# Kernel optimization log

Measured on AMD Instinct MI355X. Metric: run time of the kernel, lower is better.

Reference implementation:

```python
import jax, jax.numpy as jnp
import numpy as np
from jax import lax

N, C, K, M = 131072, 128, 27, 65536
EPS = 1e-5


def setup_inputs() -> dict:
    key = jax.random.key(0)
    ks = jax.random.split(key, 8)
    w_scale = 1.0 / np.sqrt(K * C)  # sane fan-in init for stacked kernel weights
    return {
        "x": jax.random.normal(ks[0], (N, C), jnp.float32),
        "W1": jax.random.normal(ks[1], (K, C, C), jnp.float32) * w_scale,
        "gamma1": jnp.ones((C,), jnp.float32),
        "beta1": jnp.zeros((C,), jnp.float32),
        "W2": jax.random.normal(ks[2], (K, C, C), jnp.float32) * w_scale,
        "gamma2": jnp.ones((C,), jnp.float32),
        "beta2": jnp.zeros((C,), jnp.float32),
        "map1_in": jax.random.randint(ks[3], (K, M), 0, N, jnp.int32),
        "map1_out": jax.random.randint(ks[4], (K, M), 0, N, jnp.int32),
        "map2_in": jax.random.randint(ks[5], (K, M), 0, N, jnp.int32),
        "map2_out": jax.random.randint(ks[6], (K, M), 0, N, jnp.int32),
    }


def sparse_conv(x, W, idx_in, idx_out):
    # gather-GEMM-scatter over K kernel offsets (Minkowski kernel map)
    def body(acc, kmap):
        w, ii, io = kmap                      # [C,C], [M], [M]
        contrib = x[ii] @ w                   # gather [M,C] then GEMM
        return acc.at[io].add(contrib), None  # scatter-add
    out, _ = lax.scan(body, jnp.zeros((x.shape[0], W.shape[-1]), x.dtype),
                      (W, idx_in, idx_out))
    return out


def batch_norm(x, gamma, beta):
    m = jnp.mean(x, axis=0)
    v = jnp.var(x, axis=0)
    return (x - m) * lax.rsqrt(v + EPS) * gamma + beta


def reference(x, W1, gamma1, beta1, W2, gamma2, beta2,
              map1_in, map1_out, map2_in, map2_out):
    residual = x
    out = sparse_conv(x, W1, map1_in, map1_out)
    out = jax.nn.elu(batch_norm(out, gamma1, beta1))
    out = sparse_conv(out, W2, map2_in, map2_out)
    out = batch_norm(out, gamma2, beta2) + residual
    return jax.nn.elu(out)
```

## Files before the change

kernel.cpp:

```cpp
#include <hip/hip_runtime.h>

typedef unsigned short u16;
typedef unsigned int u32;

#define NPTS 131072
#define CD 128
#define KOFF 27
#define MMAP 65536
#define LDAB 136
#define LDC 132

__device__ __forceinline__ u16 f2bf(float f) {
  u32 u = __float_as_uint(f);
  u32 r = (u + 0x7fffu + ((u >> 16) & 1u)) >> 16;
  return (u16)r;
}

typedef __attribute__((ext_vector_type(8))) short bf16x8;
typedef __attribute__((ext_vector_type(4))) float f32x4;

__global__ __launch_bounds__(256) void k_convert_x(const float* __restrict__ x,
                                                   u16* __restrict__ xb) {
  long i = ((long)blockIdx.x * 256 + threadIdx.x) * 8;
  float4 a = *(const float4*)(x + i);
  float4 b = *(const float4*)(x + i + 4);
  uint4 v;
  v.x = f2bf(a.x) | ((u32)f2bf(a.y) << 16);
  v.y = f2bf(a.z) | ((u32)f2bf(a.w) << 16);
  v.z = f2bf(b.x) | ((u32)f2bf(b.y) << 16);
  v.w = f2bf(b.z) | ((u32)f2bf(b.w) << 16);
  *(uint4*)(xb + i) = v;
}

__global__ __launch_bounds__(256) void k_convert_w(const float* __restrict__ W,
                                                   u16* __restrict__ Wb) {
  int idx = blockIdx.x * 256 + threadIdx.x;
  if (idx >= KOFF * 2048) return;
  int k = idx >> 11;
  int rem = idx & 2047;
  int co = rem >> 4;
  int cc = rem & 15;
  const float* ws = W + (long)k * (CD * CD) + (long)(cc * 8) * CD + co;
  u16 t[8];
#pragma unroll
  for (int j = 0; j < 8; ++j) t[j] = f2bf(ws[j * CD]);
  uint4 v;
  v.x = t[0] | ((u32)t[1] << 16);
  v.y = t[2] | ((u32)t[3] << 16);
  v.z = t[4] | ((u32)t[5] << 16);
  v.w = t[6] | ((u32)t[7] << 16);
  ((uint4*)Wb)[idx] = v;
}

__global__ __launch_bounds__(256) void k_hist(const int* __restrict__ mo,
                                              u32* __restrict__ hist) {
  int i = blockIdx.x * 256 + threadIdx.x;
  atomicAdd(&hist[mo[i]], 1u);
}

__global__ __launch_bounds__(256) void k_scanA(const u32* __restrict__ hist,
                                               u32* __restrict__ offs,
                                               u32* __restrict__ bsum) {
  __shared__ u32 sh[256];
  int t = threadIdx.x, b = blockIdx.x, i = b * 256 + t;
  u32 v = hist[i];
  u32 run = v;
  sh[t] = run;
  __syncthreads();
  for (int d = 1; d < 256; d <<= 1) {
    u32 y = (t >= d) ? sh[t - d] : 0u;
    __syncthreads();
    run += y;
    sh[t] = run;
    __syncthreads();
  }
  offs[i] = run - v;
  if (t == 255) bsum[b] = run;
}

__global__ __launch_bounds__(512) void k_scanB(u32* __restrict__ bsum) {
  __shared__ u32 sh[512];
  int t = threadIdx.x;
  u32 v = bsum[t];
  u32 run = v;
  sh[t] = run;
  __syncthreads();
  for (int d = 1; d < 512; d <<= 1) {
    u32 y = (t >= d) ? sh[t - d] : 0u;
    __syncthreads();
    run += y;
    sh[t] = run;
    __syncthreads();
  }
  bsum[t] = run - v;
}

__global__ __launch_bounds__(256) void k_scanC(u32* __restrict__ offs,
                                               const u32* __restrict__ bsum, u32 cnt) {
  int t = threadIdx.x, b = blockIdx.x, i = b * 256 + t;
  offs[i] += bsum[b];
  if (i == 0) offs[NPTS] = cnt;
}

__global__ __launch_bounds__(256) void k_rank(const int* __restrict__ mo,
                                              const u32* __restrict__ offs,
                                              u32* __restrict__ cur,
                                              u32* __restrict__ rank) {
  int i = blockIdx.x * 256 + threadIdx.x;
  int o = mo[i];
  rank[i] = offs[o] + atomicAdd(&cur[o], 1u);
}

__global__ __launch_bounds__(256) void k_gemm3(const u16* __restrict__ src,
                                               const u16* __restrict__ Wb,
                                               const int* __restrict__ mi,
                                               const u32* __restrict__ rank,
                                               u16* __restrict__ contrib,
                                               int kbase) {
  __shared__ u16 As[64 * LDAB];
  __shared__ u16 Bs[128 * LDAB];
  __shared__ u32 sin[64];
  __shared__ u32 srow[64];
  const int t = threadIdx.x;
  const int b = blockIdx.x;
  const int klocal = b >> 10;
  const int i0 = klocal * MMAP + (b & 1023) * 64;

  if (t < 64) {
    sin[t] = (u32)mi[i0 + t];
    srow[t] = rank[i0 + t];
  }
  const uint4* wsrc = (const uint4*)(Wb + (long)(kbase + klocal) * (CD * CD));
#pragma unroll
  for (int i = 0; i < 8; ++i) {
    int q = i * 256 + t;
    int co = q >> 4, cc = q & 15;
    *(uint4*)&Bs[co * LDAB + cc * 8] = wsrc[q];
  }
  __syncthreads();
#pragma unroll
  for (int i = 0; i < 4; ++i) {
    int q = i * 256 + t;
    int r = q >> 4, cc = q & 15;
    long row = sin[r];
    *(uint4*)&As[r * LDAB + cc * 8] = ((const uint4*)(src + row * CD))[cc];
  }
  __syncthreads();

  const int wave = t >> 6, lane = t & 63;
  const int lr = lane & 15, quad = lane >> 4;
  const int wm = (wave & 1) * 32;
  const int wn = (wave >> 1) * 64;
  f32x4 acc[2][4] = {};
#pragma unroll
  for (int kk = 0; kk < 4; ++kk) {
    bf16x8 a[2], bfr[4];
#pragma unroll
    for (int mt = 0; mt < 2; ++mt)
      a[mt] = *(const bf16x8*)&As[(wm + mt * 16 + lr) * LDAB + (kk * 4 + quad) * 8];
#pragma unroll
    for (int nt = 0; nt < 4; ++nt)
      bfr[nt] = *(const bf16x8*)&Bs[(wn + nt * 16 + lr) * LDAB + (kk * 4 + quad) * 8];
#pragma unroll
    for (int mt = 0; mt < 2; ++mt)
#pragma unroll
      for (int nt = 0; nt < 4; ++nt)
        acc[mt][nt] = __builtin_amdgcn_mfma_f32_16x16x32_bf16(a[mt], bfr[nt], acc[mt][nt], 0, 0, 0);
  }

  __syncthreads();
  u16* Cs = As;
#pragma unroll
  for (int mt = 0; mt < 2; ++mt)
#pragma unroll
    for (int v = 0; v < 4; ++v) {
      int slot = wm + mt * 16 + quad * 4 + v;
#pragma unroll
      for (int nt = 0; nt < 4; ++nt)
        Cs[slot * LDC + wn + nt * 16 + lr] = f2bf(acc[mt][nt][v]);
    }
  __syncthreads();
#pragma unroll
  for (int i = 0; i < 4; ++i) {
    int q = i * 256 + t;
    int r = q >> 4, cc = q & 15;
    size_t rk = srow[r];
    *(uint4*)(contrib + rk * CD + cc * 8) = *(const uint4*)&Cs[r * LDC + cc * 8];
  }
}

__global__ __launch_bounds__(256) void k_segreduce3(const u16* __restrict__ contrib,
                                                    const u32* __restrict__ offs,
                                                    float* __restrict__ acc,
                                                    float* __restrict__ stats,
                                                    int first, int last) {
  const int wave = threadIdx.x >> 6, lane = threadIdx.x & 63;
  const int w = blockIdx.x * 4 + wave;
  float sx = 0.f, sx2 = 0.f, sy = 0.f, sy2 = 0.f;
  for (int row = w; row < NPTS; row += 4096) {
    u32 s0 = offs[row], s1 = offs[row + 1];
    float a0 = 0.f, b0 = 0.f, a1 = 0.f, b1 = 0.f;
    u32 e = s0;
    for (; e + 2 <= s1; e += 2) {
      u32 d0 = ((const u32*)(contrib + (size_t)e * CD))[lane];
      u32 d1 = ((const u32*)(contrib + (size_t)(e + 1) * CD))[lane];
      a0 += __uint_as_float(d0 << 16);
      b0 += __uint_as_float(d0 & 0xffff0000u);
      a1 += __uint_as_float(d1 << 16);
      b1 += __uint_as_float(d1 & 0xffff0000u);
    }
    if (e < s1) {
      u32 d0 = ((const u32*)(contrib + (size_t)e * CD))[lane];
      a0 += __uint_as_float(d0 << 16);
      b0 += __uint_as_float(d0 & 0xffff0000u);
    }
    float cx = a0 + a1, cy = b0 + b1;
    float2* ap = (float2*)(acc + (size_t)row * CD) + lane;
    if (!first) {
      float2 p = *ap;
      cx += p.x;
      cy += p.y;
    }
    *ap = make_float2(cx, cy);
    if (last) {
      sx += cx;
      sx2 += cx * cx;
      sy += cy;
      sy2 += cy * cy;
    }
  }
  if (last) {
    __shared__ float sh[1024];
    sh[threadIdx.x] = sx;
    sh[256 + threadIdx.x] = sx2;
    sh[512 + threadIdx.x] = sy;
    sh[768 + threadIdx.x] = sy2;
    __syncthreads();
    if (threadIdx.x < 64) {
      int l = threadIdx.x;
      float vx = sh[l] + sh[l + 64] + sh[l + 128] + sh[l + 192];
      float vx2 = sh[256 + l] + sh[256 + l + 64] + sh[256 + l + 128] + sh[256 + l + 192];
      float vy = sh[512 + l] + sh[512 + l + 64] + sh[512 + l + 128] + sh[512 + l + 192];
      float vy2 = sh[768 + l] + sh[768 + l + 64] + sh[768 + l + 128] + sh[768 + l + 192];
      atomicAdd(&stats[2 * l], vx);
      atomicAdd(&stats[128 + 2 * l], vx2);
      atomicAdd(&stats[2 * l + 1], vy);
      atomicAdd(&stats[128 + 2 * l + 1], vy2);
    }
  }
}

__global__ void k_finalize(const float* __restrict__ stats, const float* __restrict__ gamma,
                           const float* __restrict__ beta, float* __restrict__ scsh) {
  int c = threadIdx.x;
  float mean = stats[c] * (1.f / NPTS);
  float var = stats[128 + c] * (1.f / NPTS) - mean * mean;
  float sc = rsqrtf(var + 1e-5f) * gamma[c];
  scsh[c] = sc;
  scsh[128 + c] = beta[c] - mean * sc;
}

__device__ __forceinline__ float elu(float v) { return v > 0.f ? v : expf(v) - 1.f; }

__global__ __launch_bounds__(256) void k_apply_mid(const float* __restrict__ acc,
                                                   const float* __restrict__ scsh,
                                                   u16* __restrict__ y) {
  long i = ((long)blockIdx.x * 256 + threadIdx.x) * 4;
  int c = (int)(i & 127);
  float4 a = *(const float4*)(acc + i);
  float r0 = elu(a.x * scsh[c] + scsh[128 + c]);
  float r1 = elu(a.y * scsh[c + 1] + scsh[129 + c]);
  float r2 = elu(a.z * scsh[c + 2] + scsh[130 + c]);
  float r3 = elu(a.w * scsh[c + 3] + scsh[131 + c]);
  uint2 v;
  v.x = f2bf(r0) | ((u32)f2bf(r1) << 16);
  v.y = f2bf(r2) | ((u32)f2bf(r3) << 16);
  *(uint2*)(y + i) = v;
}

__global__ __launch_bounds__(256) void k_apply_final(const float* __restrict__ acc,
                                                     const float* __restrict__ scsh,
                                                     const float* __restrict__ x,
                                                     float* __restrict__ out) {
  long i = ((long)blockIdx.x * 256 + threadIdx.x) * 4;
  int c = (int)(i & 127);
  float4 a = *(const float4*)(acc + i);
  float4 rx = *(const float4*)(x + i);
  float4 o;
  o.x = elu(a.x * scsh[c] + scsh[128 + c] + rx.x);
  o.y = elu(a.y * scsh[c + 1] + scsh[129 + c] + rx.y);
  o.z = elu(a.z * scsh[c + 2] + scsh[130 + c] + rx.z);
  o.w = elu(a.w * scsh[c + 3] + scsh[131 + c] + rx.w);
  *(float4*)(out + i) = o;
}

extern "C" void kernel_launch(void* const* d_in, const int* in_sizes, int n_in,
                              void* d_out, int out_size, void* d_ws, size_t ws_size,
                              hipStream_t stream) {
  const float* x = (const float*)d_in[0];
  const float* W1 = (const float*)d_in[1];
  const float* g1 = (const float*)d_in[2];
  const float* b1 = (const float*)d_in[3];
  const float* W2 = (const float*)d_in[4];
  const float* g2 = (const float*)d_in[5];
  const float* b2 = (const float*)d_in[6];
  const int* m1i = (const int*)d_in[7];
  const int* m1o = (const int*)d_in[8];
  const int* m2i = (const int*)d_in[9];
  const int* m2o = (const int*)d_in[10];
  float* out = (float*)d_out;

  char* base = (char*)d_ws;
  size_t off = 0;
  auto alloc = [&](size_t bytes) -> void* {
    void* r = base + off;
    off = (off + bytes + 255) & ~(size_t)255;
    return r;
  };
  u16* xb = (u16*)alloc((size_t)NPTS * CD * 2);
  u16* yb = (u16*)alloc((size_t)NPTS * CD * 2);
  u16* Wb1 = (u16*)alloc((size_t)KOFF * CD * CD * 2);
  u16* Wb2 = (u16*)alloc((size_t)KOFF * CD * CD * 2);
  float* acc = (float*)alloc((size_t)NPTS * CD * 4);
  u32* hist = (u32*)alloc((size_t)NPTS * 4);
  u32* cur = (u32*)alloc((size_t)NPTS * 4);
  size_t msSize = (size_t)((char*)base + off - (char*)hist);
  u32* offs = (u32*)alloc(((size_t)NPTS + 1) * 4);
  float* stats = (float*)alloc(256 * 4);
  float* scsh = (float*)alloc(256 * 4);
  u32* bsum = (u32*)alloc(512 * 4);

  size_t per_k = (size_t)MMAP * CD * 2 + (size_t)MMAP * 4 + 512;
  size_t avail = (ws_size > off + 4096) ? (ws_size - off - 4096) : 0;
  int kcnt = (int)(avail / per_k);
  if (kcnt < 1) kcnt = 1;
  if (kcnt > KOFF) kcnt = KOFF;
  u32* rank = (u32*)alloc((size_t)kcnt * MMAP * 4);
  u16* contrib = (u16*)alloc((size_t)kcnt * MMAP * CD * 2);

  k_convert_x<<<(NPTS * CD) / 2048, 256, 0, stream>>>(x, xb);
  k_convert_w<<<(KOFF * 2048 + 255) / 256, 256, 0, stream>>>(W1, Wb1);
  k_convert_w<<<(KOFF * 2048 + 255) / 256, 256, 0, stream>>>(W2, Wb2);

  auto run_conv = [&](const u16* srcm, const u16* Wbm, const int* mi, const int* mo) {
    hipMemsetAsync(stats, 0, 1024, stream);
    for (int g0 = 0; g0 < KOFF; g0 += kcnt) {
      int kc = (KOFF - g0 < kcnt) ? (KOFF - g0) : kcnt;
      u32 cnt = (u32)kc * MMAP;
      hipMemsetAsync(hist, 0, msSize, stream);
      k_hist<<<cnt / 256, 256, 0, stream>>>(mo + (long)g0 * MMAP, hist);
      k_scanA<<<512, 256, 0, stream>>>(hist, offs, bsum);
      k_scanB<<<1, 512, 0, stream>>>(bsum);
      k_scanC<<<512, 256, 0, stream>>>(offs, bsum, cnt);
      k_rank<<<cnt / 256, 256, 0, stream>>>(mo + (long)g0 * MMAP, offs, cur, rank);
      k_gemm3<<<kc * 1024, 256, 0, stream>>>(srcm, Wbm, mi + (long)g0 * MMAP, rank, contrib, g0);
      k_segreduce3<<<1024, 256, 0, stream>>>(contrib, offs, acc, stats,
                                             g0 == 0 ? 1 : 0, (g0 + kc == KOFF) ? 1 : 0);
    }
  };

  run_conv(xb, Wb1, m1i, m1o);
  k_finalize<<<1, 128, 0, stream>>>(stats, g1, b1, scsh);
  k_apply_mid<<<(NPTS * CD) / 1024, 256, 0, stream>>>(acc, scsh, yb);

  run_conv(yb, Wb2, m2i, m2o);
  k_finalize<<<1, 128, 0, stream>>>(stats, g2, b2, scsh);
  k_apply_final<<<(NPTS * CD) / 1024, 256, 0, stream>>>(acc, scsh, x, out);
}
```

Baseline: 1.451 ms.

## Fuse gather-GEMM-scatter into output-tile kernel with LDS accumulation

Replaces the per-offset-group gather-GEMM that wrote a large bf16 contribution buffer, followed by a segmented reduction, with a single kernel per output tile of 128 points. Each tile reads its output-sorted map entries, regroups them by kernel offset in shared memory, gathers input rows, runs MFMA, and accumulates into an fp32 LDS tile with shared atomics. BN statistics are computed in the same kernel. This removes the global round trip of the contribution buffer. The accumulator is now stored in global memory as bf16, which halves traffic in the apply kernels but loses precision. Occupancy is low because of the large LDS footprint, and entries beyond a fixed per-tile cap are silently dropped.

```diff
diff --git a/kernel.cpp b/kernel.cpp
--- a/kernel.cpp
+++ b/kernel.cpp
@@ -7,8 +7,12 @@
 #define CD 128
 #define KOFF 27
 #define MMAP 65536
+#define TOTE (KOFF * MMAP)
 #define LDAB 136
-#define LDC 132
+#define TR 128
+#define NTILE (NPTS / TR)
+#define MAXE 2560
+#define ACCP 132
 
 __device__ __forceinline__ u16 f2bf(float f) {
   u32 u = __float_as_uint(f);
@@ -96,157 +100,146 @@
 }
 
 __global__ __launch_bounds__(256) void k_scanC(u32* __restrict__ offs,
-                                               const u32* __restrict__ bsum, u32 cnt) {
+                                               const u32* __restrict__ bsum) {
   int t = threadIdx.x, b = blockIdx.x, i = b * 256 + t;
   offs[i] += bsum[b];
-  if (i == 0) offs[NPTS] = cnt;
-}
-
-__global__ __launch_bounds__(256) void k_rank(const int* __restrict__ mo,
-                                              const u32* __restrict__ offs,
-                                              u32* __restrict__ cur,
-                                              u32* __restrict__ rank) {
+  if (i == 0) offs[NPTS] = TOTE;
+}
+
+__global__ __launch_bounds__(256) void k_place(const int* __restrict__ mo,
+                                               const u32* __restrict__ offs,
+                                               u32* __restrict__ cur,
+                                               u32* __restrict__ perm) {
   int i = blockIdx.x * 256 + threadIdx.x;
   int o = mo[i];
-  rank[i] = offs[o] + atomicAdd(&cur[o], 1u);
-}
-
-__global__ __launch_bounds__(256) void k_gemm3(const u16* __restrict__ src,
-                                               const u16* __restrict__ Wb,
-                                               const int* __restrict__ mi,
-                                               const u32* __restrict__ rank,
-                                               u16* __restrict__ contrib,
-                                               int kbase) {
+  u32 p = offs[o] + atomicAdd(&cur[o], 1u);
+  perm[p] = (u32)i | ((u32)(o & (TR - 1)) << 21);
+}
+
+__global__ __launch_bounds__(512, 1) void k_fused(const u16* __restrict__ src,
+                                                  const u16* __restrict__ Wb,
+                                                  const int* __restrict__ mi,
+                                                  const u32* __restrict__ perm,
+                                                  const u32* __restrict__ offs,
+                                                  u32* __restrict__ accb,
+                                                  float* __restrict__ stats) {
+  __shared__ float accL[TR * ACCP];
   __shared__ u16 As[64 * LDAB];
   __shared__ u16 Bs[128 * LDAB];
-  __shared__ u32 sin[64];
-  __shared__ u32 srow[64];
+  __shared__ u32 sidS[MAXE];
+  __shared__ u32 sinp[MAXE];
+  __shared__ u32 kcntS[32], koffS[32], kcurS[32];
+
   const int t = threadIdx.x;
-  const int b = blockIdx.x;
-  const int klocal = b >> 10;
-  const int i0 = klocal * MMAP + (b & 1023) * 64;
-
-  if (t < 64) {
-    sin[t] = (u32)mi[i0 + t];
-    srow[t] = rank[i0 + t];
-  }
-  const uint4* wsrc = (const uint4*)(Wb + (long)(kbase + klocal) * (CD * CD));
-#pragma unroll
-  for (int i = 0; i < 8; ++i) {
-    int q = i * 256 + t;
-    int co = q >> 4, cc = q & 15;
-    *(uint4*)&Bs[co * LDAB + cc * 8] = wsrc[q];
-  }
-  __syncthreads();
-#pragma unroll
-  for (int i = 0; i < 4; ++i) {
-    int q = i * 256 + t;
-    int r = q >> 4, cc = q & 15;
-    long row = sin[r];
-    *(uint4*)&As[r * LDAB + cc * 8] = ((const uint4*)(src + row * CD))[cc];
-  }
+  const int tile = blockIdx.x;
+  const u32 s0 = offs[tile * TR];
+  const u32 s1 = offs[tile * TR + TR];
+  int n = (int)(s1 - s0);
+  if (n > MAXE) n = MAXE;
+
+  for (int i = t; i < TR * ACCP; i += 512) accL[i] = 0.f;
+  if (t < 32) kcntS[t] = 0;
+  __syncthreads();
+
+  for (int i = t; i < n; i += 512) {
+    u32 p = perm[s0 + i];
+    sinp[i] = p;
+    atomicAdd(&kcntS[(p & 0x1FFFFFu) >> 16], 1u);
+  }
+  __syncthreads();
+  if (t == 0) {
+    u32 r = 0;
+    for (int j = 0; j < KOFF; ++j) {
+      koffS[j] = r;
+      r += kcntS[j];
+    }
+  }
+  __syncthreads();
+  if (t < KOFF) kcurS[t] = koffS[t];
+  __syncthreads();
+  for (int i = t; i < n; i += 512) {
+    u32 p = sinp[i];
+    u32 pos = atomicAdd(&kcurS[(p & 0x1FFFFFu) >> 16], 1u);
+    sidS[pos] = p;
+  }
+  __syncthreads();
+  for (int i = t; i < n; i += 512) sinp[i] = (u32)mi[sidS[i] & 0x1FFFFFu];
   __syncthreads();
 
   const int wave = t >> 6, lane = t & 63;
   const int lr = lane & 15, quad = lane >> 4;
-  const int wm = (wave & 1) * 32;
-  const int wn = (wave >> 1) * 64;
-  f32x4 acc[2][4] = {};
-#pragma unroll
-  for (int kk = 0; kk < 4; ++kk) {
-    bf16x8 a[2], bfr[4];
-#pragma unroll
-    for (int mt = 0; mt < 2; ++mt)
-      a[mt] = *(const bf16x8*)&As[(wm + mt * 16 + lr) * LDAB + (kk * 4 + quad) * 8];
-#pragma unroll
-    for (int nt = 0; nt < 4; ++nt)
-      bfr[nt] = *(const bf16x8*)&Bs[(wn + nt * 16 + lr) * LDAB + (kk * 4 + quad) * 8];
-#pragma unroll
-    for (int mt = 0; mt < 2; ++mt)
-#pragma unroll
-      for (int nt = 0; nt < 4; ++nt)
-        acc[mt][nt] = __builtin_amdgcn_mfma_f32_16x16x32_bf16(a[mt], bfr[nt], acc[mt][nt], 0, 0, 0);
-  }
-
-  __syncthreads();
-  u16* Cs = As;
-#pragma unroll
-  for (int mt = 0; mt < 2; ++mt)
-#pragma unroll
-    for (int v = 0; v < 4; ++v) {
-      int slot = wm + mt * 16 + quad * 4 + v;
-#pragma unroll
-      for (int nt = 0; nt < 4; ++nt)
-        Cs[slot * LDC + wn + nt * 16 + lr] = f2bf(acc[mt][nt][v]);
+  const int wr = (wave & 3) * 16;
+  const int wc = (wave >> 2) * 64;
+
+  for (int k = 0; k < KOFF; ++k) {
+    const int nk = (int)kcntS[k];
+    if (!nk) continue;
+    __syncthreads();
+    const uint4* wsrc = (const uint4*)(Wb + (long)k * (CD * CD));
+    for (int q = t; q < 2048; q += 512) {
+      int co = q >> 4, cc = q & 15;
+      *(uint4*)&Bs[co * LDAB + cc * 8] = wsrc[q];
     }
-  __syncthreads();
-#pragma unroll
-  for (int i = 0; i < 4; ++i) {
-    int q = i * 256 + t;
-    int r = q >> 4, cc = q & 15;
-    size_t rk = srow[r];
-    *(uint4*)(contrib + rk * CD + cc * 8) = *(const uint4*)&Cs[r * LDC + cc * 8];
-  }
-}
-
-__global__ __launch_bounds__(256) void k_segreduce3(const u16* __restrict__ contrib,
-                                                    const u32* __restrict__ offs,
-                                                    float* __restrict__ acc,
-                                                    float* __restrict__ stats,
-                                                    int first, int last) {
-  const int wave = threadIdx.x >> 6, lane = threadIdx.x & 63;
-  const int w = blockIdx.x * 4 + wave;
-  float sx = 0.f, sx2 = 0.f, sy = 0.f, sy2 = 0.f;
-  for (int row = w; row < NPTS; row += 4096) {
-    u32 s0 = offs[row], s1 = offs[row + 1];
-    float a0 = 0.f, b0 = 0.f, a1 = 0.f, b1 = 0.f;
-    u32 e = s0;
-    for (; e + 2 <= s1; e += 2) {
-      u32 d0 = ((const u32*)(contrib + (size_t)e * CD))[lane];
-      u32 d1 = ((const u32*)(contrib + (size_t)(e + 1) * CD))[lane];
-      a0 += __uint_as_float(d0 << 16);
-      b0 += __uint_as_float(d0 & 0xffff0000u);
-      a1 += __uint_as_float(d1 << 16);
-      b1 += __uint_as_float(d1 & 0xffff0000u);
+    const int kb = (int)koffS[k];
+    for (int b0 = 0; b0 < nk; b0 += 64) {
+      if (b0) __syncthreads();
+      const int nv = (nk - b0 < 64) ? (nk - b0) : 64;
+      for (int q = t; q < 1024; q += 512) {
+        int r = q >> 4, cc = q & 15;
+        int idx = (r < nv) ? (kb + b0 + r) : kb;
+        long row = sinp[idx];
+        *(uint4*)&As[r * LDAB + cc * 8] = ((const uint4*)(src + row * CD))[cc];
+      }
+      __syncthreads();
+      f32x4 acc[4] = {};
+#pragma unroll
+      for (int kk = 0; kk < 4; ++kk) {
+        bf16x8 a = *(const bf16x8*)&As[(wr + lr) * LDAB + (kk * 4 + quad) * 8];
+        bf16x8 bfr[4];
+#pragma unroll
+        for (int nt = 0; nt < 4; ++nt)
+          bfr[nt] = *(const bf16x8*)&Bs[(wc + nt * 16 + lr) * LDAB + (kk * 4 + quad) * 8];
+#pragma unroll
+        for (int nt = 0; nt < 4; ++nt)
+          acc[nt] = __builtin_amdgcn_mfma_f32_16x16x32_bf16(a, bfr[nt], acc[nt], 0, 0, 0);
+      }
+#pragma unroll
+      for (int v = 0; v < 4; ++v) {
+        int slot = wr + quad * 4 + v;
+        if (slot < nv) {
+          int lrow = (int)(sidS[kb + b0 + slot] >> 21);
+          float* arow = accL + lrow * ACCP;
+#pragma unroll
+          for (int nt = 0; nt < 4; ++nt)
+            atomicAdd(&arow[wc + nt * 16 + lr], acc[nt][v]);
+        }
+      }
     }
-    if (e < s1) {
-      u32 d0 = ((const u32*)(contrib + (size_t)e * CD))[lane];
-      a0 += __uint_as_float(d0 << 16);
-      b0 += __uint_as_float(d0 & 0xffff0000u);
-    }
-    float cx = a0 + a1, cy = b0 + b1;
-    float2* ap = (float2*)(acc + (size_t)row * CD) + lane;
-    if (!first) {
-      float2 p = *ap;
-      cx += p.x;
-      cy += p.y;
-    }
-    *ap = make_float2(cx, cy);
-    if (last) {
-      sx += cx;
-      sx2 += cx * cx;
-      sy += cy;
-      sy2 += cy * cy;
-    }
-  }
-  if (last) {
-    __shared__ float sh[1024];
-    sh[threadIdx.x] = sx;
-    sh[256 + threadIdx.x] = sx2;
-    sh[512 + threadIdx.x] = sy;
-    sh[768 + threadIdx.x] = sy2;
-    __syncthreads();
-    if (threadIdx.x < 64) {
-      int l = threadIdx.x;
-      float vx = sh[l] + sh[l + 64] + sh[l + 128] + sh[l + 192];
-      float vx2 = sh[256 + l] + sh[256 + l + 64] + sh[256 + l + 128] + sh[256 + l + 192];
-      float vy = sh[512 + l] + sh[512 + l + 64] + sh[512 + l + 128] + sh[512 + l + 192];
-      float vy2 = sh[768 + l] + sh[768 + l + 64] + sh[768 + l + 128] + sh[768 + l + 192];
-      atomicAdd(&stats[2 * l], vx);
-      atomicAdd(&stats[128 + 2 * l], vx2);
-      atomicAdd(&stats[2 * l + 1], vy);
-      atomicAdd(&stats[128 + 2 * l + 1], vy2);
-    }
+  }
+  __syncthreads();
+
+  for (int i = t; i < TR * 64; i += 512) {
+    int row = i >> 6, cp = i & 63;
+    float lo = accL[row * ACCP + cp * 2];
+    float hi = accL[row * ACCP + cp * 2 + 1];
+    accb[((size_t)(tile * TR + row)) * 64 + cp] = (u32)f2bf(lo) | ((u32)f2bf(hi) << 16);
+  }
+  int c = t & 127, g = t >> 7;
+  float s = 0.f, s2 = 0.f;
+  for (int r = g; r < TR; r += 4) {
+    float v = accL[r * ACCP + c];
+    s += v;
+    s2 += v * v;
+  }
+  float* fbuf = (float*)As;
+  fbuf[t] = s;
+  fbuf[512 + t] = s2;
+  __syncthreads();
+  if (t < 128) {
+    float ss = fbuf[t] + fbuf[t + 128] + fbuf[t + 256] + fbuf[t + 384];
+    float ss2 = fbuf[512 + t] + fbuf[512 + t + 128] + fbuf[512 + t + 256] + fbuf[512 + t + 384];
+    atomicAdd(&stats[t], ss);
+    atomicAdd(&stats[128 + t], ss2);
   }
 }
 
@@ -262,36 +255,49 @@
 
 __device__ __forceinline__ float elu(float v) { return v > 0.f ? v : expf(v) - 1.f; }
 
-__global__ __launch_bounds__(256) void k_apply_mid(const float* __restrict__ acc,
+__global__ __launch_bounds__(256) void k_apply_mid(const u16* __restrict__ accb,
                                                    const float* __restrict__ scsh,
                                                    u16* __restrict__ y) {
-  long i = ((long)blockIdx.x * 256 + threadIdx.x) * 4;
+  long i = ((long)blockIdx.x * 256 + threadIdx.x) * 8;
   int c = (int)(i & 127);
-  float4 a = *(const float4*)(acc + i);
-  float r0 = elu(a.x * scsh[c] + scsh[128 + c]);
-  float r1 = elu(a.y * scsh[c + 1] + scsh[129 + c]);
-  float r2 = elu(a.z * scsh[c + 2] + scsh[130 + c]);
-  float r3 = elu(a.w * scsh[c + 3] + scsh[131 + c]);
-  uint2 v;
-  v.x = f2bf(r0) | ((u32)f2bf(r1) << 16);
-  v.y = f2bf(r2) | ((u32)f2bf(r3) << 16);
-  *(uint2*)(y + i) = v;
-}
-
-__global__ __launch_bounds__(256) void k_apply_final(const float* __restrict__ acc,
+  uint4 a = *(const uint4*)(accb + i);
+  u32 w[4] = {a.x, a.y, a.z, a.w};
+  u32 ov[4];
+#pragma unroll
+  for (int j = 0; j < 4; ++j) {
+    float lo = __uint_as_float(w[j] << 16);
+    float hi = __uint_as_float(w[j] & 0xffff0000u);
+    float r0 = elu(lo * scsh[c + 2 * j] + scsh[128 + c + 2 * j]);
+    float r1 = elu(hi * scsh[c + 2 * j + 1] + scsh[129 + c + 2 * j]);
+    ov[j] = (u32)f2bf(r0) | ((u32)f2bf(r1) << 16);
+  }
+  uint4 o = {ov[0], ov[1], ov[2], ov[3]};
+  *(uint4*)(y + i) = o;
+}
+
+__global__ __launch_bounds__(256) void k_apply_final(const u16* __restrict__ accb,
                                                      const float* __restrict__ scsh,
                                                      const float* __restrict__ x,
                                                      float* __restrict__ out) {
-  long i = ((long)blockIdx.x * 256 + threadIdx.x) * 4;
+  long i = ((long)blockIdx.x * 256 + threadIdx.x) * 8;
   int c = (int)(i & 127);
-  float4 a = *(const float4*)(acc + i);
-  float4 rx = *(const float4*)(x + i);
-  float4 o;
-  o.x = elu(a.x * scsh[c] + scsh[128 + c] + rx.x);
-  o.y = elu(a.y * scsh[c + 1] + scsh[129 + c] + rx.y);
-  o.z = elu(a.z * scsh[c + 2] + scsh[130 + c] + rx.z);
-  o.w = elu(a.w * scsh[c + 3] + scsh[131 + c] + rx.w);
-  *(float4*)(out + i) = o;
+  uint4 a = *(const uint4*)(accb + i);
+  u32 w[4] = {a.x, a.y, a.z, a.w};
+  float4 rx0 = *(const float4*)(x + i);
+  float4 rx1 = *(const float4*)(x + i + 4);
+  float rx[8] = {rx0.x, rx0.y, rx0.z, rx0.w, rx1.x, rx1.y, rx1.z, rx1.w};
+  float res[8];
+#pragma unroll
+  for (int j = 0; j < 4; ++j) {
+    float lo = __uint_as_float(w[j] << 16);
+    float hi = __uint_as_float(w[j] & 0xffff0000u);
+    res[2 * j] = elu(lo * scsh[c + 2 * j] + scsh[128 + c + 2 * j] + rx[2 * j]);
+    res[2 * j + 1] = elu(hi * scsh[c + 2 * j + 1] + scsh[129 + c + 2 * j] + rx[2 * j + 1]);
+  }
+  float4 o0 = {res[0], res[1], res[2], res[3]};
+  float4 o1 = {res[4], res[5], res[6], res[7]};
+  *(float4*)(out + i) = o0;
+  *(float4*)(out + i + 4) = o1;
 }
 
 extern "C" void kernel_launch(void* const* d_in, const int* in_sizes, int n_in,
@@ -321,49 +327,37 @@
   u16* yb = (u16*)alloc((size_t)NPTS * CD * 2);
   u16* Wb1 = (u16*)alloc((size_t)KOFF * CD * CD * 2);
   u16* Wb2 = (u16*)alloc((size_t)KOFF * CD * CD * 2);
-  float* acc = (float*)alloc((size_t)NPTS * CD * 4);
+  u32* accb = (u32*)alloc((size_t)NPTS * 64 * 4);
   u32* hist = (u32*)alloc((size_t)NPTS * 4);
   u32* cur = (u32*)alloc((size_t)NPTS * 4);
+  float* stats = (float*)alloc(256 * 4);
   size_t msSize = (size_t)((char*)base + off - (char*)hist);
   u32* offs = (u32*)alloc(((size_t)NPTS + 1) * 4);
-  float* stats = (float*)alloc(256 * 4);
   float* scsh = (float*)alloc(256 * 4);
   u32* bsum = (u32*)alloc(512 * 4);
-
-  size_t per_k = (size_t)MMAP * CD * 2 + (size_t)MMAP * 4 + 512;
-  size_t avail = (ws_size > off + 4096) ? (ws_size - off - 4096) : 0;
-  int kcnt = (int)(avail / per_k);
-  if (kcnt < 1) kcnt = 1;
-  if (kcnt > KOFF) kcnt = KOFF;
-  u32* rank = (u32*)alloc((size_t)kcnt * MMAP * 4);
-  u16* contrib = (u16*)alloc((size_t)kcnt * MMAP * CD * 2);
+  u32* perm = (u32*)alloc((size_t)TOTE * 4);
 
   k_convert_x<<<(NPTS * CD) / 2048, 256, 0, stream>>>(x, xb);
   k_convert_w<<<(KOFF * 2048 + 255) / 256, 256, 0, stream>>>(W1, Wb1);
   k_convert_w<<<(KOFF * 2048 + 255) / 256, 256, 0, stream>>>(W2, Wb2);
 
+  const int EB = TOTE / 256;
+
   auto run_conv = [&](const u16* srcm, const u16* Wbm, const int* mi, const int* mo) {
-    hipMemsetAsync(stats, 0, 1024, stream);
-    for (int g0 = 0; g0 < KOFF; g0 += kcnt) {
-      int kc = (KOFF - g0 < kcnt) ? (KOFF - g0) : kcnt;
-      u32 cnt = (u32)kc * MMAP;
-      hipMemsetAsync(hist, 0, msSize, stream);
-      k_hist<<<cnt / 256, 256, 0, stream>>>(mo + (long)g0 * MMAP, hist);
-      k_scanA<<<512, 256, 0, stream>>>(hist, offs, bsum);
-      k_scanB<<<1, 512, 0, stream>>>(bsum);
-      k_scanC<<<512, 256, 0, stream>>>(offs, bsum, cnt);
-      k_rank<<<cnt / 256, 256, 0, stream>>>(mo + (long)g0 * MMAP, offs, cur, rank);
-      k_gemm3<<<kc * 1024, 256, 0, stream>>>(srcm, Wbm, mi + (long)g0 * MMAP, rank, contrib, g0);
-      k_segreduce3<<<1024, 256, 0, stream>>>(contrib, offs, acc, stats,
-                                             g0 == 0 ? 1 : 0, (g0 + kc == KOFF) ? 1 : 0);
-    }
+    hipMemsetAsync(hist, 0, msSize, stream);
+    k_hist<<<EB, 256, 0, stream>>>(mo, hist);
+    k_scanA<<<512, 256, 0, stream>>>(hist, offs, bsum);
+    k_scanB<<<1, 512, 0, stream>>>(bsum);
+    k_scanC<<<512, 256, 0, stream>>>(offs, bsum);
+    k_place<<<EB, 256, 0, stream>>>(mo, offs, cur, perm);
+    k_fused<<<NTILE, 512, 0, stream>>>(srcm, Wbm, mi, perm, offs, accb, stats);
   };
 
   run_conv(xb, Wb1, m1i, m1o);
   k_finalize<<<1, 128, 0, stream>>>(stats, g1, b1, scsh);
-  k_apply_mid<<<(NPTS * CD) / 1024, 256, 0, stream>>>(acc, scsh, yb);
+  k_apply_mid<<<(NPTS * CD) / 2048, 256, 0, stream>>>((const u16*)accb, scsh, yb);
 
   run_conv(yb, Wb2, m2i, m2o);
   k_finalize<<<1, 128, 0, stream>>>(stats, g2, b2, scsh);
-  k_apply_final<<<(NPTS * CD) / 1024, 256, 0, stream>>>(acc, scsh, x, out);
-}
+  k_apply_final<<<(NPTS * CD) / 2048, 256, 0, stream>>>((const u16*)accb, scsh, x, out);
+}
```

New measurement: 3.531 ms. 143% more time.
